# Kernel optimization log

Measured on AMD Instinct MI355X. Metric: run time of the kernel, lower is better.

Reference implementation:

```python
import jax, jax.numpy as jnp
import numpy as np

B, T, F, H, K = 512, 128, 256, 512, 3

def setup_inputs() -> dict:
    key = jax.random.key(0)
    ks = jax.random.split(key, 8)
    x = jax.random.normal(ks[0], (B, T, F), dtype=jnp.float32)
    theta = jnp.ones((F,), dtype=jnp.float32)                 # selector logits
    Wx = jax.random.normal(ks[1], (F, H), dtype=jnp.float32) * 0.1
    Wh = jax.random.normal(ks[2], (H, H), dtype=jnp.float32) * 0.1
    b = jnp.zeros((H,), dtype=jnp.float32)
    c = jax.random.normal(ks[3], (H, K), dtype=jnp.float32)   # fuzzy centers
    sigma = jnp.ones((H, K), dtype=jnp.float32)               # fuzzy widths
    q = jax.random.normal(ks[4], (H, K), dtype=jnp.float32)   # rule consequents
    Wc = jax.random.normal(ks[5], (H, 1), dtype=jnp.float32) * 0.05  # classifier
    bc = jnp.zeros((1,), dtype=jnp.float32)
    return dict(x=x, theta=theta, Wx=Wx, Wh=Wh, b=b, c=c, sigma=sigma, q=q, Wc=Wc, bc=bc)


def reference(x, theta, Wx, Wh, b, c, sigma, q, Wc, bc):
    weights = jax.nn.sigmoid(theta)                 # [F]
    xf = x * weights                                # [B,T,F]
    # x_t @ Wx is used twice per step (for z_t and new_info); precompute once for all t.
    xw = jnp.einsum('btf,fh->bth', xf, Wx)          # [B,T,H]
    new_info = jnp.tanh(xw)                         # [B,T,H]
    inv_den = 1.0 / (2.0 * sigma ** 2 + 1e-8)       # [H,K]

    def step(h, inp):
        xw_t, new_t = inp                           # [B,H], [B,H]
        z = xw_t + h @ Wh + b                       # [B,H]
        mu = jnp.exp(-(z[..., None] - c) ** 2 * inv_den)   # [B,H,K]
        g = jax.nn.sigmoid(jnp.sum(mu * q, axis=-1) / (jnp.sum(mu, axis=-1) + 1e-8))
        h = (1.0 - g) * h + g * new_t
        return h, None

    h0 = jnp.zeros((x.shape[0], Wh.shape[0]), dtype=x.dtype)
    h, _ = jax.lax.scan(step, h0, (jnp.swapaxes(xw, 0, 1), jnp.swapaxes(new_info, 0, 1)))
    logits = h @ Wc + bc                            # [B,1]
    return logits, weights
```

## Files before the change

kernel.cpp:

```cpp
#include <hip/hip_runtime.h>
#include <hip/hip_bf16.h>


#define B_  512
#define T_  128
#define F_  256
#define H_  512
#define LOG2E 1.4426950408889634f

#define XW_T_STRIDE 262144

typedef __attribute__((ext_vector_type(8))) short short8;
typedef __attribute__((ext_vector_type(4))) float float4v;
typedef __attribute__((ext_vector_type(4))) int int4i;

__device__ inline ushort f2bf(float f) {
  __hip_bfloat16 h = __float2bfloat16(f);
  return *reinterpret_cast<ushort*>(&h);
}
__device__ inline float bf2f(unsigned u) { return __uint_as_float(u << 16); }
__device__ inline float fexp2(float x) { return __builtin_amdgcn_exp2f(x); }
__device__ inline float frcp(float x) { return __builtin_amdgcn_rcpf(x); }

#define WS_W2I8 67108864
#define WS_WXF  67371008
#define WS_GP8  67633152
#define WS_BVEC 67649536
#define WS_WCV  67651584
#define WS_SCOL 67653632
#define WS_WTS  67657728

__global__ void prep_small(const float* __restrict__ theta,
                           const float* __restrict__ b,
                           const float* __restrict__ c,
                           const float* __restrict__ sigma,
                           const float* __restrict__ q,
                           const float* __restrict__ Wc,
                           float* __restrict__ out_w,
                           float* __restrict__ gp8,
                           float* __restrict__ bvec,
                           float* __restrict__ wcv,
                           float* __restrict__ wts) {
  const int i = threadIdx.x;
  if (i < F_) {
    float w = 1.f / (1.f + __expf(-theta[i]));
    out_w[i] = w;
    wts[i] = w;
  }
  {
    float a[3], cc[3], qq[3];
#pragma unroll
    for (int k = 0; k < 3; ++k) {
      float s = sigma[i * 3 + k];
      cc[k] = c[i * 3 + k];
      a[k] = -LOG2E / (2.f * s * s + 1e-8f);
      qq[k] = q[i * 3 + k];
    }
    gp8[i * 8 + 0] = cc[0];
    gp8[i * 8 + 1] = cc[1];
    gp8[i * 8 + 2] = cc[2];
    gp8[i * 8 + 3] = a[0];
    gp8[i * 8 + 4] = a[1];
    gp8[i * 8 + 5] = a[2];
    gp8[i * 8 + 6] = __uint_as_float((unsigned)f2bf(qq[0]) |
                                     ((unsigned)f2bf(qq[1]) << 16));
    gp8[i * 8 + 7] = __uint_as_float((unsigned)f2bf(qq[2]));
    bvec[i] = b[i];
    wcv[i] = Wc[i];
  }
}

__global__ __launch_bounds__(256) void prep_weights(
    const float* __restrict__ Wh, const float* __restrict__ Wx,
    int* __restrict__ W2, ushort* __restrict__ WxF,
    float* __restrict__ scol) {
  __shared__ float lds[16544];
  const int t = threadIdx.x;

  if (blockIdx.x < 32) {
    const int nb = blockIdx.x;
    const int cc = t & 15, rg = t >> 4;
    float m = 0.f;
#pragma unroll
    for (int s = 0; s < 32; ++s)
      m = fmaxf(m, fabsf(Wh[(rg + s * 16) * H_ + nb * 16 + cc]));
    lds[rg * 16 + cc] = m;
    __syncthreads();
    if (t < 16) {
      float mm = lds[t];
#pragma unroll
      for (int s = 1; s < 16; ++s) mm = fmaxf(mm, lds[s * 16 + t]);
      mm = fmaxf(mm, 1e-20f);
      scol[nb * 16 + t] = mm / (127.f * 127.f);
      lds[256 + t] = 127.f / mm;
    }
    __syncthreads();
    const int lane = t & 63, dw = t >> 6;
    const int n = nb * 16 + (lane & 15);
    const float iv = lds[256 + (lane & 15)];
#pragma unroll
    for (int kt = 0; kt < 8; ++kt) {
      int pk = 0;
#pragma unroll
      for (int jj = 0; jj < 4; ++jj) {
        const int k = kt * 64 + ((lane >> 4) << 4) + dw * 4 + jj;
        int qv = (int)rintf(Wh[k * H_ + n] * iv);
        qv = min(127, max(-127, qv));
        pk |= (qv & 255) << (8 * jj);
      }
      W2[((kt * 32 + nb) * 64 + lane) * 4 + dw] = pk;
    }
  } else {
    const int kt = blockIdx.x - 32;
#pragma unroll
    for (int it = 0; it < 16; ++it) {
      const int lin = (it * 256 + t) * 4;
      const float4 v = *(const float4*)(Wx + kt * 32 * H_ + lin);
      const int f = lin >> 9, n0 = lin & 511;
      lds[f * 517 + n0 + 0] = v.x;
      lds[f * 517 + n0 + 1] = v.y;
      lds[f * 517 + n0 + 2] = v.z;
      lds[f * 517 + n0 + 3] = v.w;
    }
    __syncthreads();
#pragma unroll
    for (int it = 0; it < 8; ++it) {
      const int o = (it * 256 + t) * 8;
      const int lane = (o >> 3) & 63, nb = o >> 9;
      const int n = nb * 16 + (lane & 15), fb = (lane >> 4) << 3;
      ushort v[8];
#pragma unroll
      for (int j = 0; j < 8; ++j) v[j] = f2bf(lds[(fb + j) * 517 + n]);
      *(short8*)(WxF + kt * 16384 + o) = *(short8*)v;
    }
  }
}

__global__ __launch_bounds__(256, 1) void gemm1_kernel(
    const float* __restrict__ x, const float* __restrict__ wts,
    const ushort* __restrict__ WxF, ushort* __restrict__ xw2) {
  __shared__ ushort A[64 * 264];
  const int tid = threadIdx.x;
  const int lane = tid & 63, wg = tid >> 6;
  const int col16 = lane & 15, quad = lane >> 4;
  const int tt = blockIdx.x, bb = blockIdx.y;

  {
    const float4 wv = *(const float4*)(wts + lane * 4);
#pragma unroll
    for (int it = 0; it < 16; ++it) {
      const int row = it * 4 + wg;
      float4 xv = *(const float4*)(x + ((size_t)(bb * 64 + row) * T_ + tt) * F_ + lane * 4);
      ushort4 o;
      o.x = f2bf(xv.x * wv.x);
      o.y = f2bf(xv.y * wv.y);
      o.z = f2bf(xv.z * wv.z);
      o.w = f2bf(xv.w * wv.w);
      *(ushort4*)&A[row * 264 + lane * 4] = o;
    }
  }
  __syncthreads();

  const float4v zero = {0.f, 0.f, 0.f, 0.f};
#pragma unroll
  for (int nn = 0; nn < 2; ++nn) {
    float4v acc[16];
#pragma unroll
    for (int i = 0; i < 16; ++i) acc[i] = zero;
#pragma unroll
    for (int kt = 0; kt < 8; ++kt) {
      short8 af = *(const short8*)&A[(wg * 16 + col16) * 264 + kt * 32 + quad * 8];
      short8 bfv[16];
#pragma unroll
      for (int nt = 0; nt < 16; ++nt)
        bfv[nt] = *(const short8*)(WxF + ((kt * 32 + nn * 16 + nt) * 64 + lane) * 8);
#pragma unroll
      for (int nt = 0; nt < 16; ++nt)
        acc[nt] = __builtin_amdgcn_mfma_f32_16x16x32_bf16(af, bfv[nt], acc[nt], 0, 0, 0);
    }
#pragma unroll
    for (int nt = 0; nt < 16; ++nt) {
      ushort2 lo, hi;
      lo.x = f2bf(acc[nt][0]);
      lo.y = f2bf(acc[nt][1]);
      hi.x = f2bf(acc[nt][2]);
      hi.y = f2bf(acc[nt][3]);
      const int bg0 = bb * 32 + wg * 8 + quad * 2;
      const size_t off0 =
          (((size_t)tt * 256 + bg0) * 8 + nn * 4 + (nt >> 2)) * 128 +
          ((nt & 3) * 16 + col16) * 2;
      *(ushort2*)(xw2 + off0) = lo;
      *(ushort2*)(xw2 + off0 + 1024) = hi;
    }
  }
}

__global__ __launch_bounds__(512, 2) void scan4_kernel(
    const ushort* __restrict__ xw2, const int4i* __restrict__ W2,
    const float* __restrict__ gp8, const float* __restrict__ bvec,
    const float* __restrict__ wcv, const float* __restrict__ scol,
    const float* __restrict__ bc, float* __restrict__ out) {
  __shared__ int hl4[2 * 16 * 132];
  __shared__ float red[8][2];
  const int tid = threadIdx.x;
  const int lane = tid & 63, w = tid >> 6;
  const int col16 = lane & 15, quad = lane >> 4;
  const int bg = blockIdx.x;

  for (int i = tid; i < 2 * 16 * 132; i += 512) hl4[i] = 0;

  int4i bfr[8][4];
#pragma unroll
  for (int kt = 0; kt < 8; ++kt)
#pragma unroll
    for (int nt = 0; nt < 4; ++nt)
      bfr[kt][nt] = W2[(kt * 32 + w * 4 + nt) * 64 + lane];

  const int col = w * 64 + lane;
  const float bcol = bvec[col], scl = scol[col], wcl = wcv[col];
  float4v g0 = *(const float4v*)(gp8 + col * 8);
  float4v g1 = *(const float4v*)(gp8 + col * 8 + 4);
  const float c0v = g0[0], c1v = g0[1], c2v = g0[2];
  const float a0v = g0[3], a1v = g1[0], a2v = g1[1];
  unsigned p01 = __float_as_uint(g1[2]);
  const float q0v = bf2f(p01 & 0xffffu);
  const float q1v = bf2f(p01 >> 16);
  const float q2v = bf2f(__float_as_uint(g1[3]) & 0xffffu);

  const unsigned selA = (lane & 1) ? 0x07030501u : 0x02060004u;
  const unsigned selB = (lane & 2) ? 0x07060302u : 0x01000504u;

  float hreg[2] = {0.f, 0.f};

  const ushort* xwb = xw2 + ((size_t)bg * 8 + w) * 128 + lane * 2;
  unsigned xv = *(const unsigned*)xwb;
  unsigned xn;
  __syncthreads();

#pragma clang loop unroll(disable)
  for (int t = 0; t < T_; ++t) {
    const int tn = (t + 1) & 127;
    xn = *(const unsigned*)(xwb + (size_t)tn * XW_T_STRIDE);

    const char* bufr = (const char*)(hl4 + (t & 1) * 2112);
    int4i acc[4];
    const int4i izero = {0, 0, 0, 0};
#pragma unroll
    for (int nt = 0; nt < 4; ++nt) acc[nt] = izero;
#pragma unroll
    for (int kt = 0; kt < 8; ++kt) {
      int4i a = *(const int4i*)(bufr + col16 * 528 + kt * 64 + quad * 16);
#pragma unroll
      for (int nt = 0; nt < 4; ++nt)
        acc[nt] = __builtin_amdgcn_mfma_i32_16x16x64_i8(a, bfr[kt][nt], acc[nt], 0, 0, 0);
    }
    int accq[2];
#pragma unroll
    for (int rg = 0; rg < 2; ++rg) {
      int t0 = __shfl(acc[0][rg], col16, 64);
      int t1 = __shfl(acc[1][rg], col16, 64);
      int t2 = __shfl(acc[2][rg], col16, 64);
      int t3 = __shfl(acc[3][rg], col16, 64);
      int sA = (quad & 1) ? t1 : t0;
      int sB = (quad & 1) ? t3 : t2;
      accq[rg] = (quad & 2) ? sB : sA;
    }

    int qb[2];
#pragma unroll
    for (int rg = 0; rg < 2; ++rg) {
      float v = __uint_as_float(rg ? (xv & 0xffff0000u) : (xv << 16));
      float z = v + bcol + (float)accq[rg] * scl;
      float e = fexp2(v * (2.f * LOG2E));
      float nw = 1.f - 2.f * frcp(1.f + e);
      float d0 = z - c0v, d1 = z - c1v, d2 = z - c2v;
      float m0 = fexp2(d0 * d0 * a0v);
      float m1 = fexp2(d1 * d1 * a1v);
      float m2 = fexp2(d2 * d2 * a2v);
      float num = m0 * q0v + m1 * q1v + m2 * q2v;
      float den = m0 + m1 + m2 + 1e-8f;
      float s = num * frcp(den);
      float gg = frcp(1.f + fexp2(-s * LOG2E));
      float h = hreg[rg] + gg * (nw - hreg[rg]);
      hreg[rg] = h;
      qb[rg] = (int)rintf(h * 127.f);
    }

    if (t < T_ - 1) {
      int pk = (qb[0] & 255) | ((qb[1] & 255) << 8);
      int p1 = __shfl_xor(pk, 1, 64);
      int Aw = __builtin_amdgcn_perm((unsigned)pk, (unsigned)p1, selA);
      int p2 = __shfl_xor(Aw, 2, 64);
      int Tw = __builtin_amdgcn_perm((unsigned)Aw, (unsigned)p2, selB);
      int* bufw = hl4 + (((t + 1) & 1) * 2112);
      bufw[(col16 & 3) * 132 + w * 16 + quad * 4 + (col16 >> 2)] = Tw;
      __syncthreads();
    }
    xv = xn;
  }

  float part[2];
#pragma unroll
  for (int rg = 0; rg < 2; ++rg) {
    part[rg] = hreg[rg] * wcl;
#pragma unroll
    for (int m = 1; m < 64; m <<= 1) part[rg] += __shfl_xor(part[rg], m, 64);
  }
  if (lane == 0) {
    red[w][0] = part[0];
    red[w][1] = part[1];
  }
  __syncthreads();
  if (tid < 2) {
    float s = bc[0];
#pragma unroll
    for (int ww = 0; ww < 8; ++ww) s += red[ww][tid];
    out[bg * 2 + tid] = s;
  }
}

extern "C" void kernel_launch(void* const* d_in, const int* in_sizes, int n_in,
                              void* d_out, int out_size, void* d_ws, size_t ws_size,
                              hipStream_t stream) {
  const float* x     = (const float*)d_in[0];
  const float* theta = (const float*)d_in[1];
  const float* Wx    = (const float*)d_in[2];
  const float* Wh    = (const float*)d_in[3];
  const float* b     = (const float*)d_in[4];
  const float* c     = (const float*)d_in[5];
  const float* sigma = (const float*)d_in[6];
  const float* q     = (const float*)d_in[7];
  const float* Wc    = (const float*)d_in[8];
  const float* bc    = (const float*)d_in[9];
  float* out = (float*)d_out;

  ushort* xw2 = (ushort*)d_ws;
  int*    W2  = (int*)((char*)d_ws + WS_W2I8);
  ushort* WxF = (ushort*)((char*)d_ws + WS_WXF);
  float*  gp8 = (float*)((char*)d_ws + WS_GP8);
  float*  bv  = (float*)((char*)d_ws + WS_BVEC);
  float*  wcv = (float*)((char*)d_ws + WS_WCV);
  float*  scl = (float*)((char*)d_ws + WS_SCOL);
  float*  wts = (float*)((char*)d_ws + WS_WTS);

  hipLaunchKernelGGL(prep_small, dim3(1), dim3(512), 0, stream,
                     theta, b, c, sigma, q, Wc, out + B_, gp8, bv, wcv, wts);
  hipLaunchKernelGGL(prep_weights, dim3(40), dim3(256), 0, stream,
                     Wh, Wx, W2, WxF, scl);
  hipLaunchKernelGGL(gemm1_kernel, dim3(128, 8), dim3(256), 0, stream,
                     x, wts, WxF, xw2);
  hipLaunchKernelGGL(scan4_kernel, dim3(256), dim3(512), 0, stream,
                     xw2, (const int4i*)W2, gp8, bv, wcv, scl, bc, out);
}
```

Measured before the change: 278.9 us.

## Shrink shared hidden-state buffer to two valid rows and simplify transpose

The per-step int8 hidden-state exchange now stores only the two real batch rows (1152 bytes per buffer) instead of a 16-row padded tile. Only lanes with col16<2 load A fragments into registers, and the other lanes keep zeros. One shuffle plus one perm and a 16-bit store replace two shuffles and two perms. This cuts LDS traffic and ALU work on the serial recurrence critical path, but adds 16-bit stores that may raise bank-conflict or alignment costs.

```diff
diff --git a/kernel.cpp b/kernel.cpp
--- a/kernel.cpp
+++ b/kernel.cpp
@@ -200,14 +200,14 @@
     const float* __restrict__ gp8, const float* __restrict__ bvec,
     const float* __restrict__ wcv, const float* __restrict__ scol,
     const float* __restrict__ bc, float* __restrict__ out) {
-  __shared__ int hl4[2 * 16 * 132];
+  __shared__ char hb[2][1152];
   __shared__ float red[8][2];
   const int tid = threadIdx.x;
   const int lane = tid & 63, w = tid >> 6;
   const int col16 = lane & 15, quad = lane >> 4;
   const int bg = blockIdx.x;
 
-  for (int i = tid; i < 2 * 16 * 132; i += 512) hl4[i] = 0;
+  for (int i = tid; i < 576; i += 512) ((int*)hb)[i] = 0;
 
   int4i bfr[8][4];
 #pragma unroll
@@ -227,10 +227,14 @@
   const float q1v = bf2f(p01 >> 16);
   const float q2v = bf2f(__float_as_uint(g1[3]) & 0xffffu);
 
-  const unsigned selA = (lane & 1) ? 0x07030501u : 0x02060004u;
-  const unsigned selB = (lane & 2) ? 0x07060302u : 0x01000504u;
+  const unsigned wsel = (lane & 1) ? 0x0501u : 0x0004u;
+  const int woff = col + ((lane & 1) ? 575 : 0);
 
   float hreg[2] = {0.f, 0.f};
+  const int4i izero = {0, 0, 0, 0};
+  int4i areg[8];
+#pragma unroll
+  for (int kt = 0; kt < 8; ++kt) areg[kt] = izero;
 
   const ushort* xwb = xw2 + ((size_t)bg * 8 + w) * 128 + lane * 2;
   unsigned xv = *(const unsigned*)xwb;
@@ -242,18 +246,22 @@
     const int tn = (t + 1) & 127;
     xn = *(const unsigned*)(xwb + (size_t)tn * XW_T_STRIDE);
 
-    const char* bufr = (const char*)(hl4 + (t & 1) * 2112);
+    if (col16 < 2) {
+      const char* abase = hb[t & 1] + col16 * 576;
+#pragma unroll
+      for (int kt = 0; kt < 8; ++kt)
+        areg[kt] = *(const int4i*)(abase + kt * 64 + (quad << 4));
+    }
+
     int4i acc[4];
-    const int4i izero = {0, 0, 0, 0};
 #pragma unroll
     for (int nt = 0; nt < 4; ++nt) acc[nt] = izero;
 #pragma unroll
-    for (int kt = 0; kt < 8; ++kt) {
-      int4i a = *(const int4i*)(bufr + col16 * 528 + kt * 64 + quad * 16);
+    for (int kt = 0; kt < 8; ++kt)
 #pragma unroll
       for (int nt = 0; nt < 4; ++nt)
-        acc[nt] = __builtin_amdgcn_mfma_i32_16x16x64_i8(a, bfr[kt][nt], acc[nt], 0, 0, 0);
-    }
+        acc[nt] = __builtin_amdgcn_mfma_i32_16x16x64_i8(areg[kt], bfr[kt][nt], acc[nt], 0, 0, 0);
+
     int accq[2];
 #pragma unroll
     for (int rg = 0; rg < 2; ++rg) {
@@ -288,12 +296,9 @@
 
     if (t < T_ - 1) {
       int pk = (qb[0] & 255) | ((qb[1] & 255) << 8);
-      int p1 = __shfl_xor(pk, 1, 64);
-      int Aw = __builtin_amdgcn_perm((unsigned)pk, (unsigned)p1, selA);
-      int p2 = __shfl_xor(Aw, 2, 64);
-      int Tw = __builtin_amdgcn_perm((unsigned)Aw, (unsigned)p2, selB);
-      int* bufw = hl4 + (((t + 1) & 1) * 2112);
-      bufw[(col16 & 3) * 132 + w * 16 + quad * 4 + (col16 >> 2)] = Tw;
+      unsigned p1 = (unsigned)__shfl_xor(pk, 1, 64);
+      unsigned v16 = __builtin_amdgcn_perm((unsigned)pk, p1, wsel);
+      *(ushort*)(hb[(t + 1) & 1] + woff) = (ushort)v16;
       __syncthreads();
     }
     xv = xn;
```

Result: faster. 272.0 us (-2.5%).
